# Performance work log

Measured on AMD Instinct MI355X. Metric: run time of the kernel, lower is better.

The kernel has to match this reference:

```python
import jax, jax.numpy as jnp
import numpy as np

NBUS = 33
B33 = [(1,2),(2,3),(3,4),(4,5),(5,6),(6,7),(7,8),(8,9),(9,10),(10,11),(11,12),(12,13),(13,14),(14,15),(15,16),(16,17),(17,18),(2,19),(19,20),(20,21),(21,22),(3,23),(23,24),(24,25),(6,26),(26,27),(27,28),(28,29),(29,30),(30,31),(31,32),(32,33)]


def setup_inputs() -> dict:
    key = jax.random.key(0)
    k1, k2, k3 = jax.random.split(key, 3)
    B, W, M, F = 32, 128, 100, 8
    N, H, GH, K = NBUS, 256, 128, 3
    rng = np.random.default_rng(0)
    br = np.array(B33) - 1
    src = np.concatenate([br[:, 0], br[:, 1]])
    dst = np.concatenate([br[:, 1], br[:, 0]])
    w_half = rng.uniform(0.5, 2.0, size=br.shape[0]).astype(np.float32)
    p = lambda *s: jnp.asarray(rng.normal(0.0, 0.02, size=s).astype(np.float32))
    z = lambda *s: jnp.zeros(s, jnp.float32)
    return {
        'r_seq': jax.random.normal(k1, (B, W, M), jnp.float32),
        'feat_seq': jax.random.normal(k2, (B, W, F), jnp.float32),
        'x_wls_seq': jax.random.normal(k3, (B, W, 2 * N), jnp.float32),
        'edge_index': jnp.asarray(np.stack([src, dst]).astype(np.int32)),
        'edge_weight': jnp.asarray(np.concatenate([w_half, w_half])),
        'pre_w': p(F + 2, GH), 'pre_b': z(GH),
        'tag_w1': p(K + 1, GH, GH), 'tag_b1': z(GH),
        'tag_w2': p(K + 1, GH, GH), 'tag_b2': z(GH),
        'post_w': p(GH, H), 'post_b': z(H),
        'tp_w1': p(M + 2 * N, H), 'tp_b1': z(H),
        'tp_w2': p(H, H), 'tp_b2': z(H),
        'gru_wih0': p(H, 3 * H), 'gru_whh0': p(H, 3 * H), 'gru_bih0': z(3 * H), 'gru_bhh0': z(3 * H),
        'gru_wih1': p(H, 3 * H), 'gru_whh1': p(H, 3 * H), 'gru_bih1': z(3 * H), 'gru_bhh1': z(3 * H),
        'fg_w': p(H, H), 'fg_b': z(H),
        'fs_w': p(H, H), 'fs_b': z(H),
        'gate_w': p(2 * H, H), 'gate_b': z(H),
        'd1_w': p(H, H), 'd1_b': z(H),
        'd2_w': p(H, 2), 'd2_b': z(2),
    }


def _gru_layer(x, wih, whh, bih, bhh):
    # x: (B, W, Din); torch GRU gate order [r, z, n]
    def step(h, xt):
        gi = xt @ wih + bih
        gh = h @ whh + bhh
        ir, iz, inn = jnp.split(gi, 3, axis=-1)
        hr, hz, hn = jnp.split(gh, 3, axis=-1)
        r = jax.nn.sigmoid(ir + hr)
        zt = jax.nn.sigmoid(iz + hz)
        n = jnp.tanh(inn + r * hn)
        h = (1.0 - zt) * n + zt * h
        return h, h
    h0 = jnp.zeros((x.shape[0], whh.shape[0]), x.dtype)
    _, ys = jax.lax.scan(step, h0, jnp.swapaxes(x, 0, 1))
    return jnp.swapaxes(ys, 0, 1)


def _forward(r_seq, feat_seq, x_wls_seq, edge_index, edge_weight,
             pre_w, pre_b, tag_w1, tag_b1, tag_w2, tag_b2, post_w, post_b,
             tp_w1, tp_b1, tp_w2, tp_b2,
             gru_wih0, gru_whh0, gru_bih0, gru_bhh0,
             gru_wih1, gru_whh1, gru_bih1, gru_bhh1,
             fg_w, fg_b, fs_w, fs_b, gate_w, gate_b,
             d1_w, d1_b, d2_w, d2_b):
    B, W, M = r_seq.shape
    N = NBUS
    # ---- spatial branch (batched TAGConv, K=3, 2 layers) ----
    va = x_wls_seq[..., :N, None]
    vm = x_wls_seq[..., N:, None]
    x_nodes = jnp.concatenate([va, vm], axis=-1)                 # (B,W,N,2)
    feat_n = jnp.broadcast_to(feat_seq[:, :, None, :], (B, W, N, feat_seq.shape[-1]))
    gin = jnp.concatenate([feat_n, x_nodes], axis=-1) @ pre_w + pre_b  # (B,W,N,GH)
    g = gin.reshape(B * W, N, gin.shape[-1])
    src, dst = edge_index[0], edge_index[1]
    # gcn_norm (no self-loops), shared across all B*W graph copies
    deg = jnp.zeros((N,), g.dtype).at[dst].add(edge_weight)
    dinv = jnp.where(deg > 0, deg ** -0.5, 0.0)
    norm = dinv[src] * edge_weight * dinv[dst]                   # (E,)

    def prop(h):  # out[i] = sum_{j->i} norm * h[j], batched over graphs
        return jnp.zeros_like(h).at[:, dst].add(h[:, src] * norm[None, :, None])

    def tag(h, Wk, b):  # TAGConv: sum_k A^k h @ W_k + b
        out = h @ Wk[0]
        hk = h
        for k in range(1, Wk.shape[0]):
            hk = prop(hk)
            out = out + hk @ Wk[k]
        return out + b

    g = jax.nn.relu(tag(g, tag_w1, tag_b1))
    g = tag(g, tag_w2, tag_b2)
    g = g.reshape(B, W, N, -1) @ post_w + post_b                 # (B,W,N,H)
    # ---- temporal branch (MLP -> 2-layer GRU); E_time=None skips MHA ----
    s = jnp.concatenate([r_seq, x_wls_seq], axis=-1)
    s = jax.nn.relu(s @ tp_w1 + tp_b1)
    s = jax.nn.relu(s @ tp_w2 + tp_b2)
    s = _gru_layer(s, gru_wih0, gru_whh0, gru_bih0, gru_bhh0)
    s = _gru_layer(s, gru_wih1, gru_whh1, gru_bih1, gru_bhh1)    # (B,W,H)
    # ---- gated fusion + decoder ----
    g_t = g @ fg_w + fg_b                                        # (B,W,N,H)
    s_t = (s @ fs_w + fs_b)[:, :, None, :]                       # (B,W,1,H)
    s_full = jnp.broadcast_to(s_t, g_t.shape)
    alpha = jax.nn.sigmoid(jnp.concatenate([g_t, s_full], axis=-1) @ gate_w + gate_b)
    u = alpha * g_t + (1.0 - alpha) * s_full
    u = jax.nn.relu(u @ d1_w + d1_b) @ d2_w + d2_b               # (B,W,N,2)
    dx = jnp.concatenate([u[..., 0], u[..., 1]], axis=-1)        # (B,W,2N)
    return x_wls_seq + dx


def reference(r_seq, feat_seq, x_wls_seq, edge_index, edge_weight,
              pre_w, pre_b, tag_w1, tag_b1, tag_w2, tag_b2, post_w, post_b,
              tp_w1, tp_b1, tp_w2, tp_b2,
              gru_wih0, gru_whh0, gru_bih0, gru_bhh0,
              gru_wih1, gru_whh1, gru_bih1, gru_bhh1,
              fg_w, fg_b, fs_w, fs_b, gate_w, gate_b,
              d1_w, d1_b, d2_w, d2_b):
    return _forward(r_seq, feat_seq, x_wls_seq, edge_index, edge_weight,
                    pre_w, pre_b, tag_w1, tag_b1, tag_w2, tag_b2, post_w, post_b,
                    tp_w1, tp_b1, tp_w2, tp_b2,
                    gru_wih0, gru_whh0, gru_bih0, gru_bhh0,
                    gru_wih1, gru_whh1, gru_bih1, gru_bhh1,
                    fg_w, fg_b, fs_w, fs_b, gate_w, gate_b,
                    d1_w, d1_b, d2_w, d2_b)
```

## Files before the change

### kernel.cpp

```cpp
#include <hip/hip_runtime.h>
#include <hip/hip_fp16.h>
#include <cmath>

#define DEV __device__ __forceinline__

typedef unsigned short ushortT;
typedef short bs8 __attribute__((ext_vector_type(8)));
typedef float f32x4 __attribute__((ext_vector_type(4)));
typedef _Float16 f16x2 __attribute__((ext_vector_type(2)));

constexpr int kBW = 4096;
constexpr int kM = 100, kF = 8, kN = 33, kH = 256, kGH = 128, kE = 64;

constexpr int OFF_ROWPTR  = 0;
constexpr int OFF_COLSRC  = 64;
constexpr int OFF_COLNORM = 128;
constexpr int OFF_C       = 192;
constexpr int OFF_WC      = 512;
constexpr int OFF_SPRE    = 33280;
constexpr int OFF_GI      = OFF_SPRE + kBW * kH;
constexpr int OFF_SFUSE   = OFF_GI + kBW * 3 * kH;
constexpr int OFF_SGATE   = OFF_SFUSE + kBW * kH;
constexpr int OFF_WQ0     = OFF_SFUSE;
constexpr int OFF_WQ1     = OFF_SFUSE + 98304;
constexpr int WB_TW1  = 0;
constexpr int WB_TW2  = 65536;
constexpr int WB_WC   = 131072;
constexpr int WB_GATE = 163840;
constexpr int WB_D1   = 229376;
constexpr int WB_TOT  = 294912;

DEV float frcp(float x) { return __builtin_amdgcn_rcpf(x); }
DEV float fsig(float x) { return frcp(1.0f + __expf(-x)); }
DEV float ftanh(float x) { float e = __expf(2.0f * x); return 1.0f - 2.0f * frcp(e + 1.0f); }

DEV ushortT f2bf(float x) {
  unsigned u = __float_as_uint(x);
  unsigned r = u + 0x7fffu + ((u >> 16) & 1u);
  return (ushortT)(r >> 16);
}
DEV float bf2f(ushortT u) { return __uint_as_float(((unsigned)u) << 16); }

DEV f32x4 mfma16(bs8 a, bs8 b, f32x4 c) {
  return __builtin_amdgcn_mfma_f32_16x16x32_bf16(a, b, c, 0, 0, 0);
}
DEV bs8 ldb(const ushortT* p) { return *reinterpret_cast<const bs8*>(p); }

#if __has_builtin(__builtin_amdgcn_fdot2)
DEV float dot2(unsigned w, unsigned hp, float acc) {
  f16x2 wv = __builtin_bit_cast(f16x2, w);
  f16x2 hv = __builtin_bit_cast(f16x2, hp);
  return __builtin_amdgcn_fdot2(wv, hv, acc, false);
}
#else
DEV float dot2(unsigned w, unsigned hp, float acc) {
  f16x2 wv = __builtin_bit_cast(f16x2, w);
  f16x2 hv = __builtin_bit_cast(f16x2, hp);
  acc = fmaf((float)wv.x, (float)hv.x, acc);
  acc = fmaf((float)wv.y, (float)hv.y, acc);
  return acc;
}
#endif

__global__ void k_prep(const int* __restrict__ ei, const float* __restrict__ ew,
                       float* __restrict__ ws) {
  if (blockIdx.x != 0 || threadIdx.x != 0) return;
  int* rowptr = (int*)(ws + OFF_ROWPTR);
  int* colsrc = (int*)(ws + OFF_COLSRC);
  float* colnorm = ws + OFF_COLNORM;
  const int* src = ei;
  const int* dst = ei + kE;
  float deg[kN]; int cnt[kN];
  for (int n = 0; n < kN; ++n) { deg[n] = 0.f; cnt[n] = 0; }
  for (int e = 0; e < kE; ++e) { deg[dst[e]] += ew[e]; cnt[dst[e]]++; }
  float dinv[kN];
  for (int n = 0; n < kN; ++n) dinv[n] = deg[n] > 0.f ? 1.0f / sqrtf(deg[n]) : 0.f;
  int pos[kN];
  int run = 0;
  for (int n = 0; n < kN; ++n) { rowptr[n] = run; pos[n] = run; run += cnt[n]; }
  rowptr[kN] = run;
  for (int e = 0; e < kE; ++e) {
    int d = dst[e];
    int p = pos[d]++;
    colsrc[p] = src[e];
    colnorm[p] = dinv[src[e]] * ew[e] * dinv[d];
  }
}

__global__ void k_wcfold(const float* __restrict__ post_w, const float* __restrict__ post_b,
                         const float* __restrict__ fg_w, const float* __restrict__ fg_b,
                         float* __restrict__ ws) {
  const int j = threadIdx.x;
  if ((int)blockIdx.x < kGH) {
    const int k = blockIdx.x;
    float a = 0.f;
    #pragma unroll 4
    for (int m = 0; m < kH; ++m) a = fmaf(post_w[k * kH + m], fg_w[m * kH + j], a);
    ws[OFF_WC + k * kH + j] = a;
  } else {
    float a = fg_b[j];
    #pragma unroll 4
    for (int m = 0; m < kH; ++m) a = fmaf(post_b[m], fg_w[m * kH + j], a);
    ws[OFF_C + j] = a;
  }
}

__global__ void k_wq(const float* __restrict__ w0, const float* __restrict__ w1,
                     float* __restrict__ ws) {
  const int idx = blockIdx.x * 256 + threadIdx.x;
  if (idx >= 2 * 98304) return;
  const int layer = idx / 98304;
  const int rem = idx - layer * 98304;
  const int p = rem / 768, j = rem - p * 768;
  const float* w = layer ? w1 : w0;
  unsigned* dst = (unsigned*)(ws + (layer ? OFF_WQ1 : OFF_WQ0));
  __half2 v = __floats2half2_rn(w[(2 * p) * 768 + j], w[(2 * p + 1) * 768 + j]);
  dst[rem] = *reinterpret_cast<unsigned*>(&v);
}

__global__ void k_wprep(const float* __restrict__ tw1, const float* __restrict__ tw2,
                        const float* __restrict__ gatew, const float* __restrict__ d1w,
                        float* __restrict__ ws) {
  const int idx = blockIdx.x * 256 + threadIdx.x;
  if (idx >= WB_TOT) return;
  ushortT* WB = (ushortT*)(ws + OFF_GI);
  float v; int dst;
  if (idx < 65536) {
    int s = idx >> 14, r = idx & 16383, k = r >> 7, col = r & 127;
    v = tw1[(s << 14) + (k << 7) + col]; dst = WB_TW1 + (s << 14) + (col << 7) + k;
  } else if (idx < 131072) {
    int i = idx - 65536; int s = i >> 14, r = i & 16383, k = r >> 7, col = r & 127;
    v = tw2[(s << 14) + (k << 7) + col]; dst = WB_TW2 + (s << 14) + (col << 7) + k;
  } else if (idx < 163840) {
    int i = idx - 131072; int k = i & 127, col = i >> 7;
    v = ws[OFF_WC + (k << 8) + col]; dst = WB_WC + (col << 7) + k;
  } else if (idx < 229376) {
    int i = idx - 163840; int k = i & 255, col = i >> 8;
    v = gatew[(k << 8) + col]; dst = WB_GATE + (col << 8) + k;
  } else {
    int i = idx - 229376; int k = i & 255, col = i >> 8;
    v = d1w[(k << 8) + col]; dst = WB_D1 + (col << 8) + k;
  }
  WB[dst] = f2bf(v);
}

__global__ __launch_bounds__(256) void k_tpmlp(
    const float* __restrict__ r_seq, const float* __restrict__ x_wls,
    const float* __restrict__ w1, const float* __restrict__ b1,
    const float* __restrict__ w2, const float* __restrict__ b2,
    float* __restrict__ sout) {
  __shared__ float inr[16][kM + 2 * kN];
  __shared__ float h1[16][kH];
  const int bw0 = blockIdx.x * 16, tid = threadIdx.x;
  #pragma unroll
  for (int r = 0; r < 16; ++r) {
    for (int c = tid; c < kM + 2 * kN; c += 256)
      inr[r][c] = (c < kM) ? r_seq[(bw0 + r) * kM + c]
                           : x_wls[(bw0 + r) * 2 * kN + (c - kM)];
  }
  __syncthreads();
  float acc[16];
  {
    const float bb = b1[tid];
    #pragma unroll
    for (int r = 0; r < 16; ++r) acc[r] = bb;
  }
  for (int k = 0; k < kM + 2 * kN; ++k) {
    const float w = w1[k * kH + tid];
    #pragma unroll
    for (int r = 0; r < 16; ++r) acc[r] = fmaf(inr[r][k], w, acc[r]);
  }
  #pragma unroll
  for (int r = 0; r < 16; ++r) h1[r][tid] = fmaxf(acc[r], 0.f);
  __syncthreads();
  {
    const float bb = b2[tid];
    #pragma unroll
    for (int r = 0; r < 16; ++r) acc[r] = bb;
  }
  #pragma unroll 2
  for (int k = 0; k < kH; ++k) {
    const float w = w2[k * kH + tid];
    #pragma unroll
    for (int r = 0; r < 16; ++r) acc[r] = fmaf(h1[r][k], w, acc[r]);
  }
  #pragma unroll
  for (int r = 0; r < 16; ++r) sout[(bw0 + r) * kH + tid] = fmaxf(acc[r], 0.f);
}

__global__ __launch_bounds__(768) void k_gigemm(
    const float* __restrict__ sin, const float* __restrict__ wih,
    const float* __restrict__ bih, float* __restrict__ gi) {
  __shared__ float sr[16][kH];
  const int bw0 = blockIdx.x * 16, tid = threadIdx.x;
  for (int i = tid; i < 16 * kH; i += 768) sr[i >> 8][i & 255] = sin[bw0 * kH + i];
  __syncthreads();
  float acc[16];
  {
    const float bb = bih[tid];
    #pragma unroll
    for (int r = 0; r < 16; ++r) acc[r] = bb;
  }
  #pragma unroll 2
  for (int k = 0; k < kH; ++k) {
    const float w = wih[k * 768 + tid];
    #pragma unroll
    for (int r = 0; r < 16; ++r) acc[r] = fmaf(sr[r][k], w, acc[r]);
  }
  #pragma unroll
  for (int r = 0; r < 16; ++r) gi[(bw0 + r) * 768 + tid] = acc[r];
}

__global__ __launch_bounds__(512, 2) void k_scan(
    const float* __restrict__ gi, const float* __restrict__ wq,
    const float* __restrict__ bhh, float* __restrict__ sout) {
  __shared__ __align__(16) unsigned hpk[2][kH / 2];
  const int b = blockIdx.x, tid = threadIdx.x;
  const int c = tid >> 1, hh = tid & 1;
  const unsigned* wqp = (const unsigned*)wq + hh * 64 * 768 + c;
  unsigned wA[64], wB[64], wC[64];
  #pragma unroll
  for (int p = 0; p < 64; ++p) {
    wA[p] = wqp[p * 768];
    wB[p] = wqp[p * 768 + 256];
    wC[p] = wqp[p * 768 + 512];
  }
  const float bR = bhh[c], bZ = bhh[kH + c], bN = bhh[2 * kH + c];
  if (tid < kH / 2) hpk[0][tid] = 0u;
  float h = 0.f;
  __syncthreads();
  const float* gbase = gi + b * 128 * 768 + c;
  for (int t = 0; t < 128; ++t) {
    const float* g = gbase + t * 768;
    const float gA = g[0], gB = g[256], gC = g[512];
    float aR0 = 0.f, aR1 = 0.f, aZ0 = 0.f, aZ1 = 0.f, aN0 = 0.f, aN1 = 0.f;
    const unsigned* hb = hpk[t & 1] + hh * 64;
    #pragma unroll
    for (int q = 0; q < 16; ++q) {
      const uint4 hp = *reinterpret_cast<const uint4*>(hb + 4 * q);
      aR0 = dot2(wA[4 * q + 0], hp.x, aR0);
      aZ0 = dot2(wB[4 * q + 0], hp.x, aZ0);
      aN0 = dot2(wC[4 * q + 0], hp.x, aN0);
      aR1 = dot2(wA[4 * q + 1], hp.y, aR1);
      aZ1 = dot2(wB[4 * q + 1], hp.y, aZ1);
      aN1 = dot2(wC[4 * q + 1], hp.y, aN1);
      aR0 = dot2(wA[4 * q + 2], hp.z, aR0);
      aZ0 = dot2(wB[4 * q + 2], hp.z, aZ0);
      aN0 = dot2(wC[4 * q + 2], hp.z, aN0);
      aR1 = dot2(wA[4 * q + 3], hp.w, aR1);
      aZ1 = dot2(wB[4 * q + 3], hp.w, aZ1);
      aN1 = dot2(wC[4 * q + 3], hp.w, aN1);
    }
    float aR = aR0 + aR1; aR += __shfl_xor(aR, 1, 64);
    float aZ = aZ0 + aZ1; aZ += __shfl_xor(aZ, 1, 64);
    float aN = aN0 + aN1; aN += __shfl_xor(aN, 1, 64);
    const float r = fsig(gA + bR + aR);
    const float z = fsig(gB + bZ + aZ);
    const float n = ftanh(fmaf(r, aN + bN, gC));
    h = (1.f - z) * n + z * h;
    if (hh == 0) reinterpret_cast<__half*>(hpk[(t + 1) & 1])[c] = __float2half(h);
    else sout[(b * 128 + t) * kH + c] = h;
    __syncthreads();
  }
}

__global__ __launch_bounds__(256) void k_fsgate(
    const float* __restrict__ s1, const float* __restrict__ fsw,
    const float* __restrict__ fsb, const float* __restrict__ gw,
    const float* __restrict__ gb, float* __restrict__ sfuse,
    float* __restrict__ sgate) {
  __shared__ float sr[16][kH], sf[16][kH];
  const int bw0 = blockIdx.x * 16, tid = threadIdx.x;
  for (int i = tid; i < 16 * kH; i += 256) sr[i >> 8][i & 255] = s1[bw0 * kH + i];
  __syncthreads();
  float acc[16];
  {
    const float bb = fsb[tid];
    #pragma unroll
    for (int r = 0; r < 16; ++r) acc[r] = bb;
  }
  #pragma unroll 2
  for (int k = 0; k < kH; ++k) {
    const float w = fsw[k * kH + tid];
    #pragma unroll
    for (int r = 0; r < 16; ++r) acc[r] = fmaf(sr[r][k], w, acc[r]);
  }
  #pragma unroll
  for (int r = 0; r < 16; ++r) { sf[r][tid] = acc[r]; sfuse[(bw0 + r) * kH + tid] = acc[r]; }
  __syncthreads();
  {
    const float bb = gb[tid];
    #pragma unroll
    for (int r = 0; r < 16; ++r) acc[r] = bb;
  }
  #pragma unroll 2
  for (int k = 0; k < kH; ++k) {
    const float w = gw[(kH + k) * kH + tid];
    #pragma unroll
    for (int r = 0; r < 16; ++r) acc[r] = fmaf(sf[r][k], w, acc[r]);
  }
  #pragma unroll
  for (int r = 0; r < 16; ++r) sgate[(bw0 + r) * kH + tid] = acc[r];
}


constexpr int SB0 = 0;
constexpr int SB1 = 36 * 136;
constexpr int S_TOT = 2 * 36 * 136;

DEV void propb(ushortT* __restrict__ dst, const ushortT* __restrict__ src,
               const int* __restrict__ rp, const int* __restrict__ cs,
               const float* __restrict__ cn) {
  for (int idx = threadIdx.x; idx < kN * 64; idx += 512) {
    const int n = idx >> 6, j2 = idx & 63;
    float a0 = 0.f, a1 = 0.f;
    const int p1 = rp[n + 1];
    for (int p = rp[n]; p < p1; ++p) {
      const unsigned v = *(const unsigned*)(src + cs[p] * 136 + 2 * j2);
      const float w = cn[p];
      a0 = fmaf(__uint_as_float(v << 16), w, a0);
      a1 = fmaf(__uint_as_float(v & 0xffff0000u), w, a1);
    }
    *(unsigned*)(dst + n * 136 + 2 * j2) = (unsigned)f2bf(a0) | ((unsigned)f2bf(a1) << 16);
  }
}

template <bool RELU>
DEV void tag_mfma(ushortT* __restrict__ Sb, const ushortT* __restrict__ WT,
                  const float* __restrict__ b, const int* __restrict__ rp,
                  const int* __restrict__ cs, const float* __restrict__ cn,
                  int wv, int lane) {
  const int lr = lane & 15, lg = lane >> 4;
  const int col = wv * 16 + lr;
  f32x4 acc[3];
  #pragma unroll
  for (int i = 0; i < 3; ++i) acc[i] = (f32x4){0.f, 0.f, 0.f, 0.f};
  #pragma unroll
  for (int s = 0; s < 4; ++s) {
    const ushortT* A = Sb + ((s & 1) ? SB1 : SB0);
    ushortT* Bn      = Sb + ((s & 1) ? SB0 : SB1);
    #pragma unroll
    for (int ks = 0; ks < 4; ++ks) {
      const int kof = ks * 32 + lg * 8;
      bs8 a0 = ldb(A + (lr) * 136 + kof);
      bs8 a1 = ldb(A + (16 + lr) * 136 + kof);
      bs8 a2 = ldb(A + (32 + lr) * 136 + kof);
      bs8 bb = ldb(WT + (s << 14) + (col << 7) + kof);
      acc[0] = mfma16(a0, bb, acc[0]);
      acc[1] = mfma16(a1, bb, acc[1]);
      acc[2] = mfma16(a2, bb, acc[2]);
    }
    if (s < 3) {
      propb(Bn, A, rp, cs, cn);
      __syncthreads();
    }
  }
  __syncthreads();
  const float bias = b[col];
  #pragma unroll
  for (int mt = 0; mt < 3; ++mt)
    #pragma unroll
    for (int r = 0; r < 4; ++r) {
      const int row = mt * 16 + lg * 4 + r;
      if (row < kN) {
        float x = acc[mt][r] + bias;
        if (RELU) x = fmaxf(x, 0.f);
        (Sb + SB0)[row * 136 + col] = f2bf(x);
      }
    }
  __syncthreads();
}

__global__ __launch_bounds__(512, 4) void k_fused(
    const float* __restrict__ feat_seq, const float* __restrict__ x_wls,
    const float* __restrict__ pre_w, const float* __restrict__ pre_b,
    const float* __restrict__ tb1, const float* __restrict__ tb2,
    const float* __restrict__ d1b, const float* __restrict__ d2w,
    const float* __restrict__ d2b, const float* __restrict__ ws,
    const float* __restrict__ sfuse, const float* __restrict__ sgate,
    float* __restrict__ out) {
  __shared__ __align__(16) ushortT S[S_TOT];
  __shared__ float sfrow[kH], sgrow[kH];
  __shared__ float xw[2 * kN];
  __shared__ float featl[kF];
  __shared__ int rp[kN + 1], cs[kE];
  __shared__ float cn[kE];
  __shared__ float part[8][48][2];
  const int tid = threadIdx.x, bw = blockIdx.x;
  const int wv = tid >> 6, lane = tid & 63;
  const int lr = lane & 15, lg = lane >> 4;
  const ushortT* WB = (const ushortT*)(ws + OFF_GI);
  ushortT* GT = S;

  if (tid < kH) sfrow[tid] = sfuse[bw * kH + tid];
  else if (tid < 2 * kH) sgrow[tid - kH] = sgate[bw * kH + (tid - kH)];
  if (tid < 2 * kN) xw[tid] = x_wls[bw * 2 * kN + tid];
  else if (tid >= 66 && tid < 66 + kF) featl[tid - 66] = feat_seq[bw * kF + (tid - 66)];
  if (tid >= 128 && tid < 128 + kN + 1) rp[tid - 128] = ((const int*)(ws + OFF_ROWPTR))[tid - 128];
  if (tid >= 192 && tid < 256) {
    cs[tid - 192] = ((const int*)(ws + OFF_COLSRC))[tid - 192];
    cn[tid - 192] = ws[OFF_COLNORM + (tid - 192)];
  }
  for (int i = tid; i < 3 * 136; i += 512) {
    S[SB0 + kN * 136 + i] = 0;
    S[SB1 + kN * 136 + i] = 0;
  }
  __syncthreads();

  for (int idx = tid; idx < kN * kGH; idx += 512) {
    const int n = idx >> 7, j = idx & 127;
    float a = pre_b[j];
    #pragma unroll
    for (int f = 0; f < kF; ++f) a = fmaf(featl[f], pre_w[f * kGH + j], a);
    a = fmaf(xw[n], pre_w[8 * kGH + j], a);
    a = fmaf(xw[kN + n], pre_w[9 * kGH + j], a);
    S[SB0 + n * 136 + j] = f2bf(a);
  }
  __syncthreads();

  tag_mfma<true >(S, WB + WB_TW1, tb1, rp, cs, cn, wv, lane);
  tag_mfma<false>(S, WB + WB_TW2, tb2, rp, cs, cn, wv, lane);

  {
    f32x4 acc[6];
    #pragma unroll
    for (int i = 0; i < 6; ++i) acc[i] = (f32x4){0.f, 0.f, 0.f, 0.f};
    #pragma unroll
    for (int ks = 0; ks < 4; ++ks) {
      const int kof = ks * 32 + lg * 8;
      bs8 a0 = ldb(S + SB0 + (lr) * 136 + kof);
      bs8 a1 = ldb(S + SB0 + (16 + lr) * 136 + kof);
      bs8 a2 = ldb(S + SB0 + (32 + lr) * 136 + kof);
      #pragma unroll
      for (int nt = 0; nt < 2; ++nt) {
        const int col = (wv * 2 + nt) * 16 + lr;
        bs8 bb = ldb(WB + WB_WC + (col << 7) + kof);
        acc[0 + nt] = mfma16(a0, bb, acc[0 + nt]);
        acc[2 + nt] = mfma16(a1, bb, acc[2 + nt]);
        acc[4 + nt] = mfma16(a2, bb, acc[4 + nt]);
      }
    }
    __syncthreads();
    #pragma unroll
    for (int mt = 0; mt < 3; ++mt)
      #pragma unroll
      for (int nt = 0; nt < 2; ++nt) {
        const int col = (wv * 2 + nt) * 16 + lr;
        const float cb = ws[OFF_C + col];
        const f32x4 v = acc[mt * 2 + nt];
        #pragma unroll
        for (int r = 0; r < 4; ++r) {
          const int row = mt * 16 + lg * 4 + r;
          if (row < kN) GT[row * 264 + col] = f2bf(v[r] + cb);
        }
      }
    __syncthreads();
  }

  {
    f32x4 acc[6];
    #pragma unroll
    for (int i = 0; i < 6; ++i) acc[i] = (f32x4){0.f, 0.f, 0.f, 0.f};
    #pragma unroll 2
    for (int ks = 0; ks < 8; ++ks) {
      const int kof = ks * 32 + lg * 8;
      const int r2 = (32 + lr) < 36 ? (32 + lr) : 35;
      bs8 a0 = ldb(GT + (lr) * 264 + kof);
      bs8 a1 = ldb(GT + (16 + lr) * 264 + kof);
      bs8 a2 = ldb(GT + r2 * 264 + kof);
      #pragma unroll
      for (int nt = 0; nt < 2; ++nt) {
        const int col = (wv * 2 + nt) * 16 + lr;
        bs8 bb = ldb(WB + WB_GATE + (col << 8) + kof);
        acc[0 + nt] = mfma16(a0, bb, acc[0 + nt]);
        acc[2 + nt] = mfma16(a1, bb, acc[2 + nt]);
        acc[4 + nt] = mfma16(a2, bb, acc[4 + nt]);
      }
    }
    #pragma unroll
    for (int mt = 0; mt < 3; ++mt)
      #pragma unroll
      for (int nt = 0; nt < 2; ++nt) {
        const int col = (wv * 2 + nt) * 16 + lr;
        const float sg = sgrow[col], sf = sfrow[col];
        #pragma unroll
        for (int r = 0; r < 4; ++r) {
          const int row = mt * 16 + lg * 4 + r;
          if (row < kN) {
            const float al = fsig(acc[mt * 2 + nt][r] + sg);
            const float gt = bf2f(GT[row * 264 + col]);
            acc[mt * 2 + nt][r] = al * gt + (1.f - al) * sf;
          }
        }
      }
    __syncthreads();
    #pragma unroll
    for (int mt = 0; mt < 3; ++mt)
      #pragma unroll
      for (int nt = 0; nt < 2; ++nt) {
        const int col = (wv * 2 + nt) * 16 + lr;
        #pragma unroll
        for (int r = 0; r < 4; ++r) {
          const int row = mt * 16 + lg * 4 + r;
          if (row < kN) GT[row * 264 + col] = f2bf(acc[mt * 2 + nt][r]);
        }
      }
    __syncthreads();
  }

  {
    f32x4 acc[6];
    #pragma unroll
    for (int i = 0; i < 6; ++i) acc[i] = (f32x4){0.f, 0.f, 0.f, 0.f};
    #pragma unroll 2
    for (int ks = 0; ks < 8; ++ks) {
      const int kof = ks * 32 + lg * 8;
      const int r2 = (32 + lr) < 36 ? (32 + lr) : 35;
      bs8 a0 = ldb(GT + (lr) * 264 + kof);
      bs8 a1 = ldb(GT + (16 + lr) * 264 + kof);
      bs8 a2 = ldb(GT + r2 * 264 + kof);
      #pragma unroll
      for (int nt = 0; nt < 2; ++nt) {
        const int col = (wv * 2 + nt) * 16 + lr;
        bs8 bb = ldb(WB + WB_D1 + (col << 8) + kof);
        acc[0 + nt] = mfma16(a0, bb, acc[0 + nt]);
        acc[2 + nt] = mfma16(a1, bb, acc[2 + nt]);
        acc[4 + nt] = mfma16(a2, bb, acc[4 + nt]);
      }
    }
    float p0[3][4], p1[3][4];
    #pragma unroll
    for (int mt = 0; mt < 3; ++mt)
      #pragma unroll
      for (int r = 0; r < 4; ++r) { p0[mt][r] = 0.f; p1[mt][r] = 0.f; }
    #pragma unroll
    for (int nt = 0; nt < 2; ++nt) {
      const int col = (wv * 2 + nt) * 16 + lr;
      const float db = d1b[col];
      const float2 dp = *reinterpret_cast<const float2*>(d2w + col * 2);
      #pragma unroll
      for (int mt = 0; mt < 3; ++mt)
        #pragma unroll
        for (int r = 0; r < 4; ++r) {
          const float v = fmaxf(acc[mt * 2 + nt][r] + db, 0.f);
          p0[mt][r] = fmaf(v, dp.x, p0[mt][r]);
          p1[mt][r] = fmaf(v, dp.y, p1[mt][r]);
        }
    }
    #pragma unroll
    for (int mt = 0; mt < 3; ++mt)
      #pragma unroll
      for (int r = 0; r < 4; ++r) {
        #pragma unroll
        for (int off = 1; off < 16; off <<= 1) {
          p0[mt][r] += __shfl_xor(p0[mt][r], off, 64);
          p1[mt][r] += __shfl_xor(p1[mt][r], off, 64);
        }
      }
    if (lr == 0) {
      #pragma unroll
      for (int mt = 0; mt < 3; ++mt)
        #pragma unroll
        for (int r = 0; r < 4; ++r) {
          const int row = mt * 16 + lg * 4 + r;
          part[wv][row][0] = p0[mt][r];
          part[wv][row][1] = p1[mt][r];
        }
    }
    __syncthreads();
    if (tid < 66) {
      const int c = tid >= 33 ? 1 : 0;
      const int n = tid - 33 * c;
      float s = d2b[c];
      #pragma unroll
      for (int w = 0; w < 8; ++w) s += part[w][n][c];
      out[bw * 66 + tid] = xw[tid] + s;
    }
  }
}

extern "C" void kernel_launch(void* const* d_in, const int* in_sizes, int n_in,
                              void* d_out, int out_size, void* d_ws, size_t ws_size,
                              hipStream_t stream) {
  const float* r_seq  = (const float*)d_in[0];
  const float* feat   = (const float*)d_in[1];
  const float* x_wls  = (const float*)d_in[2];
  const int*   eidx   = (const int*)d_in[3];
  const float* ew     = (const float*)d_in[4];
  const float* pre_w  = (const float*)d_in[5];
  const float* pre_b  = (const float*)d_in[6];
  const float* tag_w1 = (const float*)d_in[7];
  const float* tag_b1 = (const float*)d_in[8];
  const float* tag_w2 = (const float*)d_in[9];
  const float* tag_b2 = (const float*)d_in[10];
  const float* post_w = (const float*)d_in[11];
  const float* post_b = (const float*)d_in[12];
  const float* tp_w1  = (const float*)d_in[13];
  const float* tp_b1  = (const float*)d_in[14];
  const float* tp_w2  = (const float*)d_in[15];
  const float* tp_b2  = (const float*)d_in[16];
  const float* wih0   = (const float*)d_in[17];
  const float* whh0   = (const float*)d_in[18];
  const float* bih0   = (const float*)d_in[19];
  const float* bhh0   = (const float*)d_in[20];
  const float* wih1   = (const float*)d_in[21];
  const float* whh1   = (const float*)d_in[22];
  const float* bih1   = (const float*)d_in[23];
  const float* bhh1   = (const float*)d_in[24];
  const float* fg_w   = (const float*)d_in[25];
  const float* fg_b   = (const float*)d_in[26];
  const float* fs_w   = (const float*)d_in[27];
  const float* fs_b   = (const float*)d_in[28];
  const float* gate_w = (const float*)d_in[29];
  const float* gate_b = (const float*)d_in[30];
  const float* d1_w   = (const float*)d_in[31];
  const float* d1_b   = (const float*)d_in[32];
  const float* d2_w   = (const float*)d_in[33];
  const float* d2_b   = (const float*)d_in[34];
  float* ws = (float*)d_ws;
  float* outp = (float*)d_out;

  k_prep<<<1, 64, 0, stream>>>(eidx, ew, ws);
  k_wcfold<<<kGH + 1, kH, 0, stream>>>(post_w, post_b, fg_w, fg_b, ws);
  k_wq<<<768, 256, 0, stream>>>(whh0, whh1, ws);
  k_tpmlp<<<kBW / 16, 256, 0, stream>>>(r_seq, x_wls, tp_w1, tp_b1, tp_w2, tp_b2,
                                        ws + OFF_SPRE);
  k_gigemm<<<kBW / 16, 768, 0, stream>>>(ws + OFF_SPRE, wih0, bih0, ws + OFF_GI);
  k_scan<<<32, 512, 0, stream>>>(ws + OFF_GI, ws + OFF_WQ0, bhh0, ws + OFF_SPRE);
  k_gigemm<<<kBW / 16, 768, 0, stream>>>(ws + OFF_SPRE, wih1, bih1, ws + OFF_GI);
  k_scan<<<32, 512, 0, stream>>>(ws + OFF_GI, ws + OFF_WQ1, bhh1, ws + OFF_SPRE);
  k_wprep<<<(WB_TOT + 255) / 256, 256, 0, stream>>>(tag_w1, tag_w2, gate_w, d1_w, ws);
  k_fsgate<<<kBW / 16, 256, 0, stream>>>(ws + OFF_SPRE, fs_w, fs_b, gate_w, gate_b,
                                         ws + OFF_SFUSE, ws + OFF_SGATE);
  k_fused<<<kBW, 512, 0, stream>>>(feat, x_wls, pre_w, pre_b, tag_b1, tag_b2,
                                   d1_b, d2_w, d2_b, ws, ws + OFF_SFUSE,
                                   ws + OFF_SGATE, outp);
}
```

Before: 970.3 us.

## Process two graph samples per block in fused GNN kernel to share weight fragments

The fused per-sample kernel now handles two (batch,window) samples per workgroup. Each B-operand weight fragment loaded from global memory feeds MFMAs for both samples, and the propagation and barrier steps are shared across the pair. LDS row strides are changed (136→132, 264→260) and launch bounds drop to 2 blocks per CU, with half as many blocks launched. This doubles register accumulators and LDS per block, which may reduce occupancy in exchange for halving weight traffic and sync overhead per sample.

```diff
diff --git a/kernel.cpp b/kernel.cpp
--- a/kernel.cpp
+++ b/kernel.cpp
@@ -304,54 +304,72 @@
 }
 
 
+constexpr int BSTR = 132;
+constexpr int GSTR = 260;
 constexpr int SB0 = 0;
-constexpr int SB1 = 36 * 136;
-constexpr int S_TOT = 2 * 36 * 136;
-
-DEV void propb(ushortT* __restrict__ dst, const ushortT* __restrict__ src,
-               const int* __restrict__ rp, const int* __restrict__ cs,
-               const float* __restrict__ cn) {
-  for (int idx = threadIdx.x; idx < kN * 64; idx += 512) {
-    const int n = idx >> 6, j2 = idx & 63;
+constexpr int SB1 = 36 * BSTR;
+constexpr int ASTR = 2 * 36 * BSTR;
+
+DEV void propb2(ushortT* __restrict__ S, int dstoff, int srcoff,
+                const int* __restrict__ rp, const int* __restrict__ cs,
+                const float* __restrict__ cn) {
+  for (int idx = threadIdx.x; idx < 2 * kN * 66; idx += 512) {
+    const int g = idx >= kN * 66;
+    const int r = idx - g * (kN * 66);
+    const int n = r / 66, j2 = r - n * 66;
+    ushortT* base = S + g * ASTR;
     float a0 = 0.f, a1 = 0.f;
     const int p1 = rp[n + 1];
     for (int p = rp[n]; p < p1; ++p) {
-      const unsigned v = *(const unsigned*)(src + cs[p] * 136 + 2 * j2);
+      const unsigned v = *(const unsigned*)(base + srcoff + cs[p] * BSTR + 2 * j2);
       const float w = cn[p];
       a0 = fmaf(__uint_as_float(v << 16), w, a0);
       a1 = fmaf(__uint_as_float(v & 0xffff0000u), w, a1);
     }
-    *(unsigned*)(dst + n * 136 + 2 * j2) = (unsigned)f2bf(a0) | ((unsigned)f2bf(a1) << 16);
+    *(unsigned*)(base + dstoff + n * BSTR + 2 * j2) =
+        (unsigned)f2bf(a0) | ((unsigned)f2bf(a1) << 16);
   }
 }
 
 template <bool RELU>
-DEV void tag_mfma(ushortT* __restrict__ Sb, const ushortT* __restrict__ WT,
-                  const float* __restrict__ b, const int* __restrict__ rp,
-                  const int* __restrict__ cs, const float* __restrict__ cn,
-                  int wv, int lane) {
+DEV void tag_mfma2(ushortT* __restrict__ S, const ushortT* __restrict__ WT,
+                   const float* __restrict__ b, const int* __restrict__ rp,
+                   const int* __restrict__ cs, const float* __restrict__ cn,
+                   int wv, int lane) {
   const int lr = lane & 15, lg = lane >> 4;
   const int col = wv * 16 + lr;
-  f32x4 acc[3];
-  #pragma unroll
-  for (int i = 0; i < 3; ++i) acc[i] = (f32x4){0.f, 0.f, 0.f, 0.f};
+  f32x4 accA[3], accB[3];
+  #pragma unroll
+  for (int i = 0; i < 3; ++i) { accA[i] = (f32x4){0.f,0.f,0.f,0.f}; accB[i] = (f32x4){0.f,0.f,0.f,0.f}; }
   #pragma unroll
   for (int s = 0; s < 4; ++s) {
-    const ushortT* A = Sb + ((s & 1) ? SB1 : SB0);
-    ushortT* Bn      = Sb + ((s & 1) ? SB0 : SB1);
+    const int aoff = (s & 1) ? SB1 : SB0;
+    const int noff = (s & 1) ? SB0 : SB1;
     #pragma unroll
     for (int ks = 0; ks < 4; ++ks) {
       const int kof = ks * 32 + lg * 8;
-      bs8 a0 = ldb(A + (lr) * 136 + kof);
-      bs8 a1 = ldb(A + (16 + lr) * 136 + kof);
-      bs8 a2 = ldb(A + (32 + lr) * 136 + kof);
       bs8 bb = ldb(WT + (s << 14) + (col << 7) + kof);
-      acc[0] = mfma16(a0, bb, acc[0]);
-      acc[1] = mfma16(a1, bb, acc[1]);
-      acc[2] = mfma16(a2, bb, acc[2]);
+      {
+        const ushortT* A = S + aoff;
+        bs8 a0 = ldb(A + lr * BSTR + kof);
+        bs8 a1 = ldb(A + (16 + lr) * BSTR + kof);
+        bs8 a2 = ldb(A + (32 + lr) * BSTR + kof);
+        accA[0] = mfma16(a0, bb, accA[0]);
+        accA[1] = mfma16(a1, bb, accA[1]);
+        accA[2] = mfma16(a2, bb, accA[2]);
+      }
+      {
+        const ushortT* A = S + ASTR + aoff;
+        bs8 a0 = ldb(A + lr * BSTR + kof);
+        bs8 a1 = ldb(A + (16 + lr) * BSTR + kof);
+        bs8 a2 = ldb(A + (32 + lr) * BSTR + kof);
+        accB[0] = mfma16(a0, bb, accB[0]);
+        accB[1] = mfma16(a1, bb, accB[1]);
+        accB[2] = mfma16(a2, bb, accB[2]);
+      }
     }
     if (s < 3) {
-      propb(Bn, A, rp, cs, cn);
+      propb2(S, noff, aoff, rp, cs, cn);
       __syncthreads();
     }
   }
@@ -363,15 +381,17 @@
     for (int r = 0; r < 4; ++r) {
       const int row = mt * 16 + lg * 4 + r;
       if (row < kN) {
-        float x = acc[mt][r] + bias;
-        if (RELU) x = fmaxf(x, 0.f);
-        (Sb + SB0)[row * 136 + col] = f2bf(x);
-      }
-    }
-  __syncthreads();
-}
-
-__global__ __launch_bounds__(512, 4) void k_fused(
+        float x0 = accA[mt][r] + bias;
+        float x1 = accB[mt][r] + bias;
+        if (RELU) { x0 = fmaxf(x0, 0.f); x1 = fmaxf(x1, 0.f); }
+        (S + SB0)[row * BSTR + col] = f2bf(x0);
+        (S + ASTR + SB0)[row * BSTR + col] = f2bf(x1);
+      }
+    }
+  __syncthreads();
+}
+
+__global__ __launch_bounds__(512, 2) void k_fused(
     const float* __restrict__ feat_seq, const float* __restrict__ x_wls,
     const float* __restrict__ pre_w, const float* __restrict__ pre_b,
     const float* __restrict__ tb1, const float* __restrict__ tb2,
@@ -379,202 +399,261 @@
     const float* __restrict__ d2b, const float* __restrict__ ws,
     const float* __restrict__ sfuse, const float* __restrict__ sgate,
     float* __restrict__ out) {
-  __shared__ __align__(16) ushortT S[S_TOT];
-  __shared__ float sfrow[kH], sgrow[kH];
-  __shared__ float xw[2 * kN];
-  __shared__ float featl[kF];
+  __shared__ __align__(16) ushortT S[2 * ASTR];
+  __shared__ float sfrow[2][kH], sgrow[2][kH];
+  __shared__ float xw[2][2 * kN];
+  __shared__ float featl[2][kF];
   __shared__ int rp[kN + 1], cs[kE];
   __shared__ float cn[kE];
-  __shared__ float part[8][48][2];
-  const int tid = threadIdx.x, bw = blockIdx.x;
+  __shared__ float part[2][8][48][2];
+  const int tid = threadIdx.x, bw0 = blockIdx.x * 2;
   const int wv = tid >> 6, lane = tid & 63;
   const int lr = lane & 15, lg = lane >> 4;
   const ushortT* WB = (const ushortT*)(ws + OFF_GI);
-  ushortT* GT = S;
-
-  if (tid < kH) sfrow[tid] = sfuse[bw * kH + tid];
-  else if (tid < 2 * kH) sgrow[tid - kH] = sgate[bw * kH + (tid - kH)];
-  if (tid < 2 * kN) xw[tid] = x_wls[bw * 2 * kN + tid];
-  else if (tid >= 66 && tid < 66 + kF) featl[tid - 66] = feat_seq[bw * kF + (tid - 66)];
-  if (tid >= 128 && tid < 128 + kN + 1) rp[tid - 128] = ((const int*)(ws + OFF_ROWPTR))[tid - 128];
-  if (tid >= 192 && tid < 256) {
-    cs[tid - 192] = ((const int*)(ws + OFF_COLSRC))[tid - 192];
-    cn[tid - 192] = ws[OFF_COLNORM + (tid - 192)];
-  }
-  for (int i = tid; i < 3 * 136; i += 512) {
-    S[SB0 + kN * 136 + i] = 0;
-    S[SB1 + kN * 136 + i] = 0;
-  }
-  __syncthreads();
-
-  for (int idx = tid; idx < kN * kGH; idx += 512) {
-    const int n = idx >> 7, j = idx & 127;
-    float a = pre_b[j];
-    #pragma unroll
-    for (int f = 0; f < kF; ++f) a = fmaf(featl[f], pre_w[f * kGH + j], a);
-    a = fmaf(xw[n], pre_w[8 * kGH + j], a);
-    a = fmaf(xw[kN + n], pre_w[9 * kGH + j], a);
-    S[SB0 + n * 136 + j] = f2bf(a);
-  }
-  __syncthreads();
-
-  tag_mfma<true >(S, WB + WB_TW1, tb1, rp, cs, cn, wv, lane);
-  tag_mfma<false>(S, WB + WB_TW2, tb2, rp, cs, cn, wv, lane);
-
-  {
-    f32x4 acc[6];
-    #pragma unroll
-    for (int i = 0; i < 6; ++i) acc[i] = (f32x4){0.f, 0.f, 0.f, 0.f};
+
+  {
+    const int g = tid >> 8, j = tid & 255;
+    sfrow[g][j] = sfuse[(bw0 + g) * kH + j];
+    sgrow[g][j] = sgate[(bw0 + g) * kH + j];
+  }
+  if (tid < 132) {
+    const int g = tid >= 66;
+    const int i = tid - g * 66;
+    xw[g][i] = x_wls[(bw0 + g) * 2 * kN + i];
+  } else if (tid >= 132 && tid < 148) {
+    const int i = tid - 132, g = i >> 3;
+    featl[g][i & 7] = feat_seq[(bw0 + g) * kF + (i & 7)];
+  }
+  if (tid >= 192 && tid < 192 + kN + 1) rp[tid - 192] = ((const int*)(ws + OFF_ROWPTR))[tid - 192];
+  if (tid >= 256 && tid < 320) {
+    cs[tid - 256] = ((const int*)(ws + OFF_COLSRC))[tid - 256];
+    cn[tid - 256] = ws[OFF_COLNORM + (tid - 256)];
+  }
+  if (tid < 3 * BSTR) {
+    S[SB0 + kN * BSTR + tid] = 0;
+    S[SB1 + kN * BSTR + tid] = 0;
+    S[ASTR + SB0 + kN * BSTR + tid] = 0;
+    S[ASTR + SB1 + kN * BSTR + tid] = 0;
+  }
+  __syncthreads();
+
+  #pragma unroll
+  for (int g = 0; g < 2; ++g) {
+    ushortT* B0 = S + g * ASTR + SB0;
+    for (int idx = tid; idx < kN * kGH; idx += 512) {
+      const int n = idx >> 7, j = idx & 127;
+      float a = pre_b[j];
+      #pragma unroll
+      for (int f = 0; f < kF; ++f) a = fmaf(featl[g][f], pre_w[f * kGH + j], a);
+      a = fmaf(xw[g][n], pre_w[8 * kGH + j], a);
+      a = fmaf(xw[g][kN + n], pre_w[9 * kGH + j], a);
+      B0[n * BSTR + j] = f2bf(a);
+    }
+  }
+  __syncthreads();
+
+  tag_mfma2<true >(S, WB + WB_TW1, tb1, rp, cs, cn, wv, lane);
+  tag_mfma2<false>(S, WB + WB_TW2, tb2, rp, cs, cn, wv, lane);
+
+  {
+    f32x4 accA[6], accB[6];
+    #pragma unroll
+    for (int i = 0; i < 6; ++i) { accA[i] = (f32x4){0.f,0.f,0.f,0.f}; accB[i] = (f32x4){0.f,0.f,0.f,0.f}; }
     #pragma unroll
     for (int ks = 0; ks < 4; ++ks) {
       const int kof = ks * 32 + lg * 8;
-      bs8 a0 = ldb(S + SB0 + (lr) * 136 + kof);
-      bs8 a1 = ldb(S + SB0 + (16 + lr) * 136 + kof);
-      bs8 a2 = ldb(S + SB0 + (32 + lr) * 136 + kof);
-      #pragma unroll
-      for (int nt = 0; nt < 2; ++nt) {
-        const int col = (wv * 2 + nt) * 16 + lr;
-        bs8 bb = ldb(WB + WB_WC + (col << 7) + kof);
-        acc[0 + nt] = mfma16(a0, bb, acc[0 + nt]);
-        acc[2 + nt] = mfma16(a1, bb, acc[2 + nt]);
-        acc[4 + nt] = mfma16(a2, bb, acc[4 + nt]);
+      const int c0 = (wv * 2 + 0) * 16 + lr, c1 = (wv * 2 + 1) * 16 + lr;
+      bs8 bb0 = ldb(WB + WB_WC + (c0 << 7) + kof);
+      bs8 bb1 = ldb(WB + WB_WC + (c1 << 7) + kof);
+      {
+        const ushortT* A = S + SB0;
+        bs8 a0 = ldb(A + lr * BSTR + kof);
+        bs8 a1 = ldb(A + (16 + lr) * BSTR + kof);
+        bs8 a2 = ldb(A + (32 + lr) * BSTR + kof);
+        accA[0] = mfma16(a0, bb0, accA[0]); accA[1] = mfma16(a0, bb1, accA[1]);
+        accA[2] = mfma16(a1, bb0, accA[2]); accA[3] = mfma16(a1, bb1, accA[3]);
+        accA[4] = mfma16(a2, bb0, accA[4]); accA[5] = mfma16(a2, bb1, accA[5]);
+      }
+      {
+        const ushortT* A = S + ASTR + SB0;
+        bs8 a0 = ldb(A + lr * BSTR + kof);
+        bs8 a1 = ldb(A + (16 + lr) * BSTR + kof);
+        bs8 a2 = ldb(A + (32 + lr) * BSTR + kof);
+        accB[0] = mfma16(a0, bb0, accB[0]); accB[1] = mfma16(a0, bb1, accB[1]);
+        accB[2] = mfma16(a1, bb0, accB[2]); accB[3] = mfma16(a1, bb1, accB[3]);
+        accB[4] = mfma16(a2, bb0, accB[4]); accB[5] = mfma16(a2, bb1, accB[5]);
       }
     }
     __syncthreads();
-    #pragma unroll
-    for (int mt = 0; mt < 3; ++mt)
-      #pragma unroll
-      for (int nt = 0; nt < 2; ++nt) {
-        const int col = (wv * 2 + nt) * 16 + lr;
-        const float cb = ws[OFF_C + col];
-        const f32x4 v = acc[mt * 2 + nt];
-        #pragma unroll
-        for (int r = 0; r < 4; ++r) {
-          const int row = mt * 16 + lg * 4 + r;
-          if (row < kN) GT[row * 264 + col] = f2bf(v[r] + cb);
-        }
-      }
-    __syncthreads();
-  }
-
-  {
-    f32x4 acc[6];
-    #pragma unroll
-    for (int i = 0; i < 6; ++i) acc[i] = (f32x4){0.f, 0.f, 0.f, 0.f};
-    #pragma unroll 2
-    for (int ks = 0; ks < 8; ++ks) {
-      const int kof = ks * 32 + lg * 8;
-      const int r2 = (32 + lr) < 36 ? (32 + lr) : 35;
-      bs8 a0 = ldb(GT + (lr) * 264 + kof);
-      bs8 a1 = ldb(GT + (16 + lr) * 264 + kof);
-      bs8 a2 = ldb(GT + r2 * 264 + kof);
-      #pragma unroll
-      for (int nt = 0; nt < 2; ++nt) {
-        const int col = (wv * 2 + nt) * 16 + lr;
-        bs8 bb = ldb(WB + WB_GATE + (col << 8) + kof);
-        acc[0 + nt] = mfma16(a0, bb, acc[0 + nt]);
-        acc[2 + nt] = mfma16(a1, bb, acc[2 + nt]);
-        acc[4 + nt] = mfma16(a2, bb, acc[4 + nt]);
-      }
-    }
-    #pragma unroll
-    for (int mt = 0; mt < 3; ++mt)
-      #pragma unroll
-      for (int nt = 0; nt < 2; ++nt) {
-        const int col = (wv * 2 + nt) * 16 + lr;
-        const float sg = sgrow[col], sf = sfrow[col];
-        #pragma unroll
-        for (int r = 0; r < 4; ++r) {
-          const int row = mt * 16 + lg * 4 + r;
-          if (row < kN) {
-            const float al = fsig(acc[mt * 2 + nt][r] + sg);
-            const float gt = bf2f(GT[row * 264 + col]);
-            acc[mt * 2 + nt][r] = al * gt + (1.f - al) * sf;
-          }
-        }
-      }
-    __syncthreads();
-    #pragma unroll
-    for (int mt = 0; mt < 3; ++mt)
-      #pragma unroll
-      for (int nt = 0; nt < 2; ++nt) {
-        const int col = (wv * 2 + nt) * 16 + lr;
-        #pragma unroll
-        for (int r = 0; r < 4; ++r) {
-          const int row = mt * 16 + lg * 4 + r;
-          if (row < kN) GT[row * 264 + col] = f2bf(acc[mt * 2 + nt][r]);
-        }
-      }
-    __syncthreads();
-  }
-
-  {
-    f32x4 acc[6];
-    #pragma unroll
-    for (int i = 0; i < 6; ++i) acc[i] = (f32x4){0.f, 0.f, 0.f, 0.f};
-    #pragma unroll 2
-    for (int ks = 0; ks < 8; ++ks) {
-      const int kof = ks * 32 + lg * 8;
-      const int r2 = (32 + lr) < 36 ? (32 + lr) : 35;
-      bs8 a0 = ldb(GT + (lr) * 264 + kof);
-      bs8 a1 = ldb(GT + (16 + lr) * 264 + kof);
-      bs8 a2 = ldb(GT + r2 * 264 + kof);
-      #pragma unroll
-      for (int nt = 0; nt < 2; ++nt) {
-        const int col = (wv * 2 + nt) * 16 + lr;
-        bs8 bb = ldb(WB + WB_D1 + (col << 8) + kof);
-        acc[0 + nt] = mfma16(a0, bb, acc[0 + nt]);
-        acc[2 + nt] = mfma16(a1, bb, acc[2 + nt]);
-        acc[4 + nt] = mfma16(a2, bb, acc[4 + nt]);
-      }
-    }
-    float p0[3][4], p1[3][4];
-    #pragma unroll
-    for (int mt = 0; mt < 3; ++mt)
-      #pragma unroll
-      for (int r = 0; r < 4; ++r) { p0[mt][r] = 0.f; p1[mt][r] = 0.f; }
     #pragma unroll
     for (int nt = 0; nt < 2; ++nt) {
       const int col = (wv * 2 + nt) * 16 + lr;
-      const float db = d1b[col];
-      const float2 dp = *reinterpret_cast<const float2*>(d2w + col * 2);
-      #pragma unroll
-      for (int mt = 0; mt < 3; ++mt)
-        #pragma unroll
-        for (int r = 0; r < 4; ++r) {
-          const float v = fmaxf(acc[mt * 2 + nt][r] + db, 0.f);
-          p0[mt][r] = fmaf(v, dp.x, p0[mt][r]);
-          p1[mt][r] = fmaf(v, dp.y, p1[mt][r]);
-        }
-    }
-    #pragma unroll
-    for (int mt = 0; mt < 3; ++mt)
-      #pragma unroll
-      for (int r = 0; r < 4; ++r) {
-        #pragma unroll
-        for (int off = 1; off < 16; off <<= 1) {
-          p0[mt][r] += __shfl_xor(p0[mt][r], off, 64);
-          p1[mt][r] += __shfl_xor(p1[mt][r], off, 64);
-        }
-      }
-    if (lr == 0) {
+      const float cb = ws[OFF_C + col];
       #pragma unroll
       for (int mt = 0; mt < 3; ++mt)
         #pragma unroll
         for (int r = 0; r < 4; ++r) {
           const int row = mt * 16 + lg * 4 + r;
-          part[wv][row][0] = p0[mt][r];
-          part[wv][row][1] = p1[mt][r];
+          if (row < kN) {
+            S[row * GSTR + col] = f2bf(accA[mt * 2 + nt][r] + cb);
+            (S + ASTR)[row * GSTR + col] = f2bf(accB[mt * 2 + nt][r] + cb);
+          }
         }
     }
     __syncthreads();
-    if (tid < 66) {
-      const int c = tid >= 33 ? 1 : 0;
-      const int n = tid - 33 * c;
-      float s = d2b[c];
+  }
+
+  {
+    f32x4 accA[6], accB[6];
+    #pragma unroll
+    for (int i = 0; i < 6; ++i) { accA[i] = (f32x4){0.f,0.f,0.f,0.f}; accB[i] = (f32x4){0.f,0.f,0.f,0.f}; }
+    #pragma unroll 2
+    for (int ks = 0; ks < 8; ++ks) {
+      const int kof = ks * 32 + lg * 8;
+      const int r2 = (32 + lr) < 36 ? (32 + lr) : 35;
+      const int c0 = (wv * 2 + 0) * 16 + lr, c1 = (wv * 2 + 1) * 16 + lr;
+      bs8 bb0 = ldb(WB + WB_GATE + (c0 << 8) + kof);
+      bs8 bb1 = ldb(WB + WB_GATE + (c1 << 8) + kof);
+      {
+        const ushortT* A = S;
+        bs8 a0 = ldb(A + lr * GSTR + kof);
+        bs8 a1 = ldb(A + (16 + lr) * GSTR + kof);
+        bs8 a2 = ldb(A + r2 * GSTR + kof);
+        accA[0] = mfma16(a0, bb0, accA[0]); accA[1] = mfma16(a0, bb1, accA[1]);
+        accA[2] = mfma16(a1, bb0, accA[2]); accA[3] = mfma16(a1, bb1, accA[3]);
+        accA[4] = mfma16(a2, bb0, accA[4]); accA[5] = mfma16(a2, bb1, accA[5]);
+      }
+      {
+        const ushortT* A = S + ASTR;
+        bs8 a0 = ldb(A + lr * GSTR + kof);
+        bs8 a1 = ldb(A + (16 + lr) * GSTR + kof);
+        bs8 a2 = ldb(A + r2 * GSTR + kof);
+        accB[0] = mfma16(a0, bb0, accB[0]); accB[1] = mfma16(a0, bb1, accB[1]);
+        accB[2] = mfma16(a1, bb0, accB[2]); accB[3] = mfma16(a1, bb1, accB[3]);
+        accB[4] = mfma16(a2, bb0, accB[4]); accB[5] = mfma16(a2, bb1, accB[5]);
+      }
+    }
+    #pragma unroll
+    for (int nt = 0; nt < 2; ++nt) {
+      const int col = (wv * 2 + nt) * 16 + lr;
+      const float sg0 = sgrow[0][col], sf0 = sfrow[0][col];
+      const float sg1 = sgrow[1][col], sf1 = sfrow[1][col];
       #pragma unroll
-      for (int w = 0; w < 8; ++w) s += part[w][n][c];
-      out[bw * 66 + tid] = xw[tid] + s;
+      for (int mt = 0; mt < 3; ++mt)
+        #pragma unroll
+        for (int r = 0; r < 4; ++r) {
+          const int row = mt * 16 + lg * 4 + r;
+          if (row < kN) {
+            const float al0 = fsig(accA[mt * 2 + nt][r] + sg0);
+            const float gt0 = bf2f(S[row * GSTR + col]);
+            accA[mt * 2 + nt][r] = al0 * gt0 + (1.f - al0) * sf0;
+            const float al1 = fsig(accB[mt * 2 + nt][r] + sg1);
+            const float gt1 = bf2f((S + ASTR)[row * GSTR + col]);
+            accB[mt * 2 + nt][r] = al1 * gt1 + (1.f - al1) * sf1;
+          }
+        }
+    }
+    __syncthreads();
+    #pragma unroll
+    for (int nt = 0; nt < 2; ++nt) {
+      const int col = (wv * 2 + nt) * 16 + lr;
+      #pragma unroll
+      for (int mt = 0; mt < 3; ++mt)
+        #pragma unroll
+        for (int r = 0; r < 4; ++r) {
+          const int row = mt * 16 + lg * 4 + r;
+          if (row < kN) {
+            S[row * GSTR + col] = f2bf(accA[mt * 2 + nt][r]);
+            (S + ASTR)[row * GSTR + col] = f2bf(accB[mt * 2 + nt][r]);
+          }
+        }
+    }
+    __syncthreads();
+  }
+
+  {
+    f32x4 accA[6], accB[6];
+    #pragma unroll
+    for (int i = 0; i < 6; ++i) { accA[i] = (f32x4){0.f,0.f,0.f,0.f}; accB[i] = (f32x4){0.f,0.f,0.f,0.f}; }
+    #pragma unroll 2
+    for (int ks = 0; ks < 8; ++ks) {
+      const int kof = ks * 32 + lg * 8;
+      const int r2 = (32 + lr) < 36 ? (32 + lr) : 35;
+      const int c0 = (wv * 2 + 0) * 16 + lr, c1 = (wv * 2 + 1) * 16 + lr;
+      bs8 bb0 = ldb(WB + WB_D1 + (c0 << 8) + kof);
+      bs8 bb1 = ldb(WB + WB_D1 + (c1 << 8) + kof);
+      {
+        const ushortT* A = S;
+        bs8 a0 = ldb(A + lr * GSTR + kof);
+        bs8 a1 = ldb(A + (16 + lr) * GSTR + kof);
+        bs8 a2 = ldb(A + r2 * GSTR + kof);
+        accA[0] = mfma16(a0, bb0, accA[0]); accA[1] = mfma16(a0, bb1, accA[1]);
+        accA[2] = mfma16(a1, bb0, accA[2]); accA[3] = mfma16(a1, bb1, accA[3]);
+        accA[4] = mfma16(a2, bb0, accA[4]); accA[5] = mfma16(a2, bb1, accA[5]);
+      }
+      {
+        const ushortT* A = S + ASTR;
+        bs8 a0 = ldb(A + lr * GSTR + kof);
+        bs8 a1 = ldb(A + (16 + lr) * GSTR + kof);
+        bs8 a2 = ldb(A + r2 * GSTR + kof);
+        accB[0] = mfma16(a0, bb0, accB[0]); accB[1] = mfma16(a0, bb1, accB[1]);
+        accB[2] = mfma16(a1, bb0, accB[2]); accB[3] = mfma16(a1, bb1, accB[3]);
+        accB[4] = mfma16(a2, bb0, accB[4]); accB[5] = mfma16(a2, bb1, accB[5]);
+      }
+    }
+    #pragma unroll
+    for (int g = 0; g < 2; ++g) {
+      float p0[3][4], p1[3][4];
+      #pragma unroll
+      for (int mt = 0; mt < 3; ++mt)
+        #pragma unroll
+        for (int r = 0; r < 4; ++r) { p0[mt][r] = 0.f; p1[mt][r] = 0.f; }
+      #pragma unroll
+      for (int nt = 0; nt < 2; ++nt) {
+        const int col = (wv * 2 + nt) * 16 + lr;
+        const float db = d1b[col];
+        const float2 dp = *reinterpret_cast<const float2*>(d2w + col * 2);
+        #pragma unroll
+        for (int mt = 0; mt < 3; ++mt)
+          #pragma unroll
+          for (int r = 0; r < 4; ++r) {
+            const float av = g == 0 ? accA[mt * 2 + nt][r] : accB[mt * 2 + nt][r];
+            const float v = fmaxf(av + db, 0.f);
+            p0[mt][r] = fmaf(v, dp.x, p0[mt][r]);
+            p1[mt][r] = fmaf(v, dp.y, p1[mt][r]);
+          }
+      }
+      #pragma unroll
+      for (int mt = 0; mt < 3; ++mt)
+        #pragma unroll
+        for (int r = 0; r < 4; ++r) {
+          #pragma unroll
+          for (int off = 1; off < 16; off <<= 1) {
+            p0[mt][r] += __shfl_xor(p0[mt][r], off, 64);
+            p1[mt][r] += __shfl_xor(p1[mt][r], off, 64);
+          }
+        }
+      if (lr == 0) {
+        #pragma unroll
+        for (int mt = 0; mt < 3; ++mt)
+          #pragma unroll
+          for (int r = 0; r < 4; ++r) {
+            const int row = mt * 16 + lg * 4 + r;
+            part[g][wv][row][0] = p0[mt][r];
+            part[g][wv][row][1] = p1[mt][r];
+          }
+      }
+    }
+    __syncthreads();
+    if (tid < 132) {
+      const int g = tid >= 66;
+      const int i = tid - g * 66;
+      const int c = i >= 33 ? 1 : 0;
+      const int n = i - 33 * c;
+      float sv = d2b[c];
+      #pragma unroll
+      for (int w = 0; w < 8; ++w) sv += part[g][w][n][c];
+      out[(bw0 + g) * 66 + i] = xw[g][i] + sv;
     }
   }
 }
@@ -632,7 +711,7 @@
   k_wprep<<<(WB_TOT + 255) / 256, 256, 0, stream>>>(tag_w1, tag_w2, gate_w, d1_w, ws);
   k_fsgate<<<kBW / 16, 256, 0, stream>>>(ws + OFF_SPRE, fs_w, fs_b, gate_w, gate_b,
                                          ws + OFF_SFUSE, ws + OFF_SGATE);
-  k_fused<<<kBW, 512, 0, stream>>>(feat, x_wls, pre_w, pre_b, tag_b1, tag_b2,
-                                   d1_b, d2_w, d2_b, ws, ws + OFF_SFUSE,
-                                   ws + OFF_SGATE, outp);
-}
+  k_fused<<<kBW / 2, 512, 0, stream>>>(feat, x_wls, pre_w, pre_b, tag_b1, tag_b2,
+                                       d1_b, d2_w, d2_b, ws, ws + OFF_SFUSE,
+                                       ws + OFF_SGATE, outp);
+}
```

After: 1.391 ms. +43.3%, slower.
